# Optimization experiments

Hardware: AMD Instinct MI355X
Metric: run time of the kernel (lower is better)

Reference implementation:

```python
import jax, jax.numpy as jnp
import numpy as np

SIGMA = 0.1
B = 1.0
SPATIAL_WEIGHT = 0.5
EPS = 1e-5


def setup_inputs() -> dict:
    key = jax.random.key(0)
    k1, k2 = jax.random.split(key)
    N, C, H, W = 2, 256, 64, 64
    I_features = jax.random.normal(k1, (N, C, H, W), dtype=jnp.float32)
    T_features = jax.random.normal(k2, (N, C, H, W), dtype=jnp.float32)
    return {"I_features": I_features, "T_features": T_features}


def _calc_cx(raw):
    # raw: [N, P_T, H, W]; min + exp-softmax over the target-patch axis (axis=1)
    mn = jnp.min(raw, axis=1, keepdims=True)
    rel = raw / (mn + EPS)
    w = jnp.exp((B - rel) / SIGMA)
    return w / jnp.sum(w, axis=1, keepdims=True)


def reference(I_features, T_features):
    N, C, H, W = I_features.shape
    P = H * W

    # ---- spatial branch: L2 distances on a normalized meshgrid (C=2) ----
    rows = jnp.arange(H, dtype=jnp.float32) / (H + 1)
    cols = jnp.arange(W, dtype=jnp.float32) / (W + 1)
    grid = jnp.stack(jnp.meshgrid(rows, cols, indexing="ij"))  # [2, H, W]
    g = grid.reshape(2, P)                                      # [2, P]
    sq = jnp.sum(g * g, axis=0)                                 # [P]
    d = sq[:, None] + sq[None, :] - 2.0 * (g.T @ g)             # [P_I, P_T]
    d = jnp.clip(d, 0.0)
    raw_sp = d.T.reshape(1, P, H, W)  # [1, P_T, H, W]; identical per sample
    cx_sp = _calc_cx(raw_sp)

    # ---- feature branch: cosine similarity via centered, L2-normed feats ----
    meanT = jnp.mean(T_features, axis=(0, 2, 3), keepdims=True)
    Ic = I_features - meanT
    Tc = T_features - meanT
    In = Ic / jnp.linalg.norm(Ic, axis=1, keepdims=True)
    Tn = Tc / jnp.linalg.norm(Tc, axis=1, keepdims=True)
    Iv = In.reshape(N, C, P)
    Tv = Tn.reshape(N, C, P)
    dot = jnp.einsum("ncq,ncp->nqp", Tv, Iv)  # [N, P_T, P_I]
    raw_feat = ((1.0 - dot) / 2.0).reshape(N, P, H, W)
    cx_feat = _calc_cx(raw_feat)

    # ---- combine, max over I positions, mean over T patches, -log, mean ----
    cx = (1.0 - SPATIAL_WEIGHT) * cx_feat + SPATIAL_WEIGHT * cx_sp  # [N,P,H,W]
    m = jnp.max(cx, axis=(2, 3))  # [N, P]
    m = jnp.mean(m, axis=1)       # [N]
    return jnp.mean(-jnp.log(m))
```

## Files before the change

### kernel.cpp

```cpp
#include <hip/hip_runtime.h>
#include <math.h>

#define PP 4096
#define CC 256
#define NN 2
#define NSTEP 16

typedef __attribute__((ext_vector_type(4))) float f32x4;
typedef __attribute__((ext_vector_type(8))) int i32x8;

__device__ __forceinline__ void gld_lds16(const char* g, char* l) {
    __builtin_amdgcn_global_load_lds(
        (const __attribute__((address_space(1))) unsigned int*)g,
        (__attribute__((address_space(3))) unsigned int*)l, 16, 0, 0);
}


__global__ __launch_bounds__(256) void mean_kernel(const float* __restrict__ T,
                                                   float* __restrict__ meanT,
                                                   float* __restrict__ loss_acc) {
    int c = blockIdx.x, tid = threadIdx.x;
    float s = 0.f;
    for (int n = 0; n < NN; n++) {
        const float4* Tc = (const float4*)&T[(size_t)(n * CC + c) * PP];
        for (int g = 0; g < 4; g++) {
            float4 v = Tc[tid + g * 256];
            s += (v.x + v.y) + (v.z + v.w);
        }
    }
    __shared__ float red[256];
    red[tid] = s; __syncthreads();
    for (int st = 128; st > 0; st >>= 1) {
        if (tid < st) red[tid] += red[tid + st];
        __syncthreads();
    }
    if (tid == 0) meanT[c] = red[0] * (1.0f / (NN * PP));
    if (blockIdx.x == 0 && tid < NN) loss_acc[tid] = 0.f;
}

__global__ __launch_bounds__(256) void normalize_kernel(const float* __restrict__ I,
                                                        const float* __restrict__ T,
                                                        const float* __restrict__ meanT,
                                                        char* __restrict__ InT,
                                                        char* __restrict__ TnT) {
    int pc = blockIdx.x * 32;
    int n = blockIdx.y;
    int which = blockIdx.z;
    const float* X = which ? T : I;
    char* Y = which ? TnT : InT;

    __shared__ float tile[CC][36];
    __shared__ float red[32][32];
    __shared__ float invn[32];

    int tid = threadIdx.x;
    int pl4 = tid & 7, c0 = tid >> 3;
    float sq0 = 0.f, sq1 = 0.f, sq2 = 0.f, sq3 = 0.f;
    for (int c = c0; c < CC; c += 32) {
        float m = meanT[c];
        float4 v = *(const float4*)&X[(size_t)(n * CC + c) * PP + pc + pl4 * 4];
        v.x -= m; v.y -= m; v.z -= m; v.w -= m;
        *(float4*)&tile[c][pl4 * 4] = v;
        sq0 += v.x * v.x; sq1 += v.y * v.y; sq2 += v.z * v.z; sq3 += v.w * v.w;
    }
    red[c0][pl4 * 4 + 0] = sq0;
    red[c0][pl4 * 4 + 1] = sq1;
    red[c0][pl4 * 4 + 2] = sq2;
    red[c0][pl4 * 4 + 3] = sq3;
    __syncthreads();
    if (tid < 32) {
        float s = 0.f;
        for (int k = 0; k < 32; k++) s += red[k][tid];
        invn[tid] = 1.0f / sqrtf(s);
    }
    __syncthreads();
    for (int pass = 0; pass < 8; pass++) {
        int r = pass * 4 + (tid >> 6);
        int c4 = (tid & 63) * 4;
        float in = invn[r];
        float v0 = tile[c4 + 0][r] * in;
        float v1 = tile[c4 + 1][r] * in;
        float v2 = tile[c4 + 2][r] * in;
        float v3 = tile[c4 + 3][r] * in;
        int w = __builtin_amdgcn_cvt_pk_fp8_f32(v0, v1, 0, false);
        w = __builtin_amdgcn_cvt_pk_fp8_f32(v2, v3, w, true);
        *(unsigned*)&Y[(size_t)(n * PP + pc + r) * CC + c4] = (unsigned)w;
    }
}

__global__ __launch_bounds__(1024) void cx_strip(const char* __restrict__ TnT,
                                                 const char* __restrict__ InT,
                                                 float* __restrict__ loss_acc) {
    const int strip = blockIdx.x;
    const int n = blockIdx.y;
    const int p0 = strip * 32;
    const char* __restrict__ Ab = TnT + (size_t)n * PP * CC;
    const char* __restrict__ Bb = InT + (size_t)n * PP * CC + (size_t)p0 * CC;

    __shared__ __align__(16) char Aw[16][2][4096];
    __shared__ __align__(16) char Bsm[8192];
    __shared__ float redw[16][32];
    __shared__ float inv2s[32];
    __shared__ float dwl[32];

    const int tid = threadIdx.x;
    const int l = tid & 63, wv = tid >> 6;
    const int lm = l & 15, quad = l >> 4;
    const int lr4 = l >> 4;
    const int sl = l & 15;

    const char* asrc[4];
#pragma unroll
    for (int g = 0; g < 4; g++) {
        int row = g * 4 + lr4;
        asrc[g] = Ab + (size_t)(wv * 16 + row) * 256 + ((sl ^ (row & 15)) * 16);
    }
#define STAGE_A(qs, b)                                                        \
    {                                                                         \
        char* dbase_ = &Aw[wv][b][0];                                         \
        _Pragma("unroll")                                                     \
        for (int g_ = 0; g_ < 4; g_++)                                        \
            gld_lds16(asrc[g_] + (size_t)(qs) * 65536, dbase_ + g_ * 1024);   \
    }

    int aoff[8];
#pragma unroll
    for (int kb = 0; kb < 2; kb++)
#pragma unroll
        for (int j = 0; j < 4; j++)
            aoff[kb * 4 + j] = lm * 256 +
                (((kb * 8 + j * 2 + (quad >> 1)) ^ lm) * 16) + (quad & 1) * 8;

    if (wv < 8) {
        int rB = wv * 4 + lr4;
        gld_lds16(Bb + rB * 256 + ((sl ^ (rB & 15)) * 16), &Bsm[wv * 1024]);
    }
    STAGE_A(0, 0);
    __syncthreads();

    union BU { long l[2][8]; i32x8 v[2][2]; } bfu;
#pragma unroll
    for (int ct = 0; ct < 2; ct++)
#pragma unroll
        for (int ks = 0; ks < 8; ks++) {
            int g8 = ks * 4 + quad;
            int row = ct * 16 + lm;
            bfu.l[ct][ks] = *(const long*)&Bsm[row * 256 +
                             (((g8 >> 1) ^ (row & 15)) * 16) + (g8 & 1) * 8];
        }

    float amax[2] = {-3.4e38f, -3.4e38f};
    float hc[2] = {0.f, 0.f}, c0c[2] = {0.f, 0.f};
    float ss[2] = {0.f, 0.f};
    const int qdd0 = p0 >> 8, wdd0 = (p0 >> 4) & 15;
    const int qdd1 = (p0 + 16) >> 8, wdd1 = ((p0 + 16) >> 4) & 15;

#pragma unroll 1
    for (int pass = 0; pass < 2; pass++) {
        if (pass == 1) STAGE_A(0, 0);
#pragma unroll 1
        for (int qs = 0; qs < NSTEP; qs++) {
            if (qs < NSTEP - 1) {
                STAGE_A(qs + 1, (qs + 1) & 1);
                asm volatile("s_waitcnt vmcnt(4)" ::: "memory");
            } else {
                asm volatile("s_waitcnt vmcnt(0)" ::: "memory");
            }
            __builtin_amdgcn_sched_barrier(0);

            const char* Ac = &Aw[wv][qs & 1][0];
            f32x4 acc[2] = {};
#pragma unroll
            for (int kb = 0; kb < 2; kb++) {
                union AU { long l[4]; i32x8 v; } a_;
#pragma unroll
                for (int j = 0; j < 4; j++)
                    a_.l[j] = *(const long*)&Ac[aoff[kb * 4 + j]];
#pragma unroll
                for (int ct = 0; ct < 2; ct++)
                    acc[ct] = __builtin_amdgcn_mfma_scale_f32_16x16x128_f8f6f4(
                        a_.v, bfu.v[ct][kb], acc[ct],
                        0, 0,
                        0, 0x7f7f7f7f,
                        0, 0x7f7f7f7f);
            }
            if (pass == 0) {
#pragma unroll
                for (int ct = 0; ct < 2; ct++)
#pragma unroll
                    for (int e = 0; e < 4; e++)
                        amax[ct] = fmaxf(amax[ct], acc[ct][e]);
            } else {
#pragma unroll
                for (int ct = 0; ct < 2; ct++) {
                    float s2 = 0.f;
#pragma unroll
                    for (int e = 0; e < 4; e++)
                        s2 += exp2f(fmaf(acc[ct][e], hc[ct], c0c[ct]));
                    ss[ct] += s2;
                }
                if (qs == qdd0 && wv == wdd0 && quad == (lm >> 2))
                    dwl[lm] = exp2f(fmaf(acc[0][lm & 3], hc[0], c0c[0]));
                if (qs == qdd1 && wv == wdd1 && quad == (lm >> 2))
                    dwl[16 + lm] = exp2f(fmaf(acc[1][lm & 3], hc[1], c0c[1]));
            }
        }

        if (pass == 0) {
#pragma unroll
            for (int ct = 0; ct < 2; ct++) {
                amax[ct] = fmaxf(amax[ct], __shfl_xor(amax[ct], 16));
                amax[ct] = fmaxf(amax[ct], __shfl_xor(amax[ct], 32));
                if (quad == 0) redw[wv][ct * 16 + lm] = amax[ct];
            }
            __syncthreads();
            if (tid < 32) {
                float mx = redw[0][tid];
#pragma unroll
                for (int w2 = 1; w2 < 16; w2++) mx = fmaxf(mx, redw[w2][tid]);
                float mnv = (1.0f - mx) * 0.5f;
                inv2s[tid] = 14.4269504f / (mnv + 1e-5f);
            }
            __syncthreads();
            {
                float i20 = inv2s[lm], i21 = inv2s[16 + lm];
                hc[0] = i20 * 0.5f; c0c[0] = 14.4269504f - hc[0];
                hc[1] = i21 * 0.5f; c0c[1] = 14.4269504f - hc[1];
            }
        }
    }

#pragma unroll
    for (int ct = 0; ct < 2; ct++) {
        ss[ct] += __shfl_xor(ss[ct], 16);
        ss[ct] += __shfl_xor(ss[ct], 32);
        if (quad == 0) redw[wv][ct * 16 + lm] = ss[ct];
    }
    __syncthreads();
    if (tid < 32) {
        float s = 0.f;
#pragma unroll
        for (int w2 = 0; w2 < 16; w2++) s += redw[w2][tid];
        float part = dwl[tid] / s;
        part += __shfl_xor(part, 1);
        part += __shfl_xor(part, 2);
        part += __shfl_xor(part, 4);
        part += __shfl_xor(part, 8);
        part += __shfl_xor(part, 16);
        if (tid == 0) atomicAdd(&loss_acc[n], part);
    }
#undef STAGE_A
}

__global__ void finalize_kernel(const float* __restrict__ loss_acc,
                                float* __restrict__ out) {
    float m0 = 0.5f + 0.5f * (loss_acc[0] / (float)PP);
    float m1 = 0.5f + 0.5f * (loss_acc[1] / (float)PP);
    out[0] = 0.5f * (-logf(m0) - logf(m1));
}

extern "C" void kernel_launch(void* const* d_in, const int* in_sizes, int n_in,
                              void* d_out, int out_size, void* d_ws, size_t ws_size,
                              hipStream_t stream) {
    const float* I = (const float*)d_in[0];
    const float* T = (const float*)d_in[1];
    float* out = (float*)d_out;

    char* ws = (char*)d_ws;
    const size_t SZ_F8 = (size_t)NN * PP * CC;
    char* InT = ws;
    char* TnT = ws + SZ_F8;
    float* meanT = (float*)(ws + 2 * SZ_F8);
    float* loss_acc = (float*)(ws + 2 * SZ_F8 + 32768);

    mean_kernel<<<CC, 256, 0, stream>>>(T, meanT, loss_acc);
    normalize_kernel<<<dim3(PP / 32, NN, 2), 256, 0, stream>>>(I, T, meanT, InT, TnT);
    cx_strip<<<dim3(PP / 32, NN), 1024, 0, stream>>>(TnT, InT, loss_acc);
    finalize_kernel<<<1, 1, 0, stream>>>(loss_acc, out);
}
```

Before: 105.4 us.

## Load MFMA operands directly from global into registers, dropping LDS staging

Removes the LDS double-buffer staging of A and B tiles via global_load_lds, along with the swizzled LDS reads. Each lane now loads its fp8 operand fragments straight from global memory into registers and prefetches the next step's A fragment into a register double buffer. This cuts the LDS round trip, the explicit vmcnt waits and the LDS footprint, which may help occupancy. In exchange, global loads become 8-byte per-lane accesses with less coalescing, and loop-carried latency hiding is left to the compiler.

```diff
diff --git a/kernel.cpp b/kernel.cpp
--- a/kernel.cpp
+++ b/kernel.cpp
@@ -8,12 +8,7 @@
 
 typedef __attribute__((ext_vector_type(4))) float f32x4;
 typedef __attribute__((ext_vector_type(8))) int i32x8;
-
-__device__ __forceinline__ void gld_lds16(const char* g, char* l) {
-    __builtin_amdgcn_global_load_lds(
-        (const __attribute__((address_space(1))) unsigned int*)g,
-        (__attribute__((address_space(3))) unsigned int*)l, 16, 0, 0);
-}
+typedef __attribute__((ext_vector_type(2))) int i32x2;
 
 
 __global__ __launch_bounds__(256) void mean_kernel(const float* __restrict__ T,
@@ -97,8 +92,6 @@
     const char* __restrict__ Ab = TnT + (size_t)n * PP * CC;
     const char* __restrict__ Bb = InT + (size_t)n * PP * CC + (size_t)p0 * CC;
 
-    __shared__ __align__(16) char Aw[16][2][4096];
-    __shared__ __align__(16) char Bsm[8192];
     __shared__ float redw[16][32];
     __shared__ float inv2s[32];
     __shared__ float dwl[32];
@@ -106,48 +99,19 @@
     const int tid = threadIdx.x;
     const int l = tid & 63, wv = tid >> 6;
     const int lm = l & 15, quad = l >> 4;
-    const int lr4 = l >> 4;
-    const int sl = l & 15;
-
-    const char* asrc[4];
-#pragma unroll
-    for (int g = 0; g < 4; g++) {
-        int row = g * 4 + lr4;
-        asrc[g] = Ab + (size_t)(wv * 16 + row) * 256 + ((sl ^ (row & 15)) * 16);
-    }
-#define STAGE_A(qs, b)                                                        \
-    {                                                                         \
-        char* dbase_ = &Aw[wv][b][0];                                         \
-        _Pragma("unroll")                                                     \
-        for (int g_ = 0; g_ < 4; g_++)                                        \
-            gld_lds16(asrc[g_] + (size_t)(qs) * 65536, dbase_ + g_ * 1024);   \
-    }
-
-    int aoff[8];
-#pragma unroll
-    for (int kb = 0; kb < 2; kb++)
-#pragma unroll
-        for (int j = 0; j < 4; j++)
-            aoff[kb * 4 + j] = lm * 256 +
-                (((kb * 8 + j * 2 + (quad >> 1)) ^ lm) * 16) + (quad & 1) * 8;
-
-    if (wv < 8) {
-        int rB = wv * 4 + lr4;
-        gld_lds16(Bb + rB * 256 + ((sl ^ (rB & 15)) * 16), &Bsm[wv * 1024]);
-    }
-    STAGE_A(0, 0);
-    __syncthreads();
-
-    union BU { long l[2][8]; i32x8 v[2][2]; } bfu;
+
+    union BU { i32x2 d[2][2][4]; i32x8 v[2][2]; } bf;
 #pragma unroll
     for (int ct = 0; ct < 2; ct++)
 #pragma unroll
-        for (int ks = 0; ks < 8; ks++) {
-            int g8 = ks * 4 + quad;
-            int row = ct * 16 + lm;
-            bfu.l[ct][ks] = *(const long*)&Bsm[row * 256 +
-                             (((g8 >> 1) ^ (row & 15)) * 16) + (g8 & 1) * 8];
-        }
+        for (int kb = 0; kb < 2; kb++)
+#pragma unroll
+            for (int j = 0; j < 4; j++)
+                bf.d[ct][kb][j] = *(const i32x2*)(Bb + (ct * 16 + lm) * 256 +
+                                                  kb * 128 + j * 32 + quad * 8);
+
+    const char* Abase = Ab + (size_t)(wv * 16 + lm) * 256 + quad * 8;
+    union AU { i32x2 d[2][4]; i32x8 v[2]; };
 
     float amax[2] = {-3.4e38f, -3.4e38f};
     float hc[2] = {0.f, 0.f}, c0c[2] = {0.f, 0.f};
@@ -157,33 +121,35 @@
 
 #pragma unroll 1
     for (int pass = 0; pass < 2; pass++) {
-        if (pass == 1) STAGE_A(0, 0);
-#pragma unroll 1
+        AU cur, nxt;
+#pragma unroll
+        for (int kb = 0; kb < 2; kb++)
+#pragma unroll
+            for (int j = 0; j < 4; j++)
+                cur.d[kb][j] = *(const i32x2*)(Abase + kb * 128 + j * 32);
+
+#pragma unroll 2
         for (int qs = 0; qs < NSTEP; qs++) {
             if (qs < NSTEP - 1) {
-                STAGE_A(qs + 1, (qs + 1) & 1);
-                asm volatile("s_waitcnt vmcnt(4)" ::: "memory");
-            } else {
-                asm volatile("s_waitcnt vmcnt(0)" ::: "memory");
-            }
-            __builtin_amdgcn_sched_barrier(0);
-
-            const char* Ac = &Aw[wv][qs & 1][0];
+#pragma unroll
+                for (int kb = 0; kb < 2; kb++)
+#pragma unroll
+                    for (int j = 0; j < 4; j++)
+                        nxt.d[kb][j] = *(const i32x2*)(Abase +
+                            (size_t)(qs + 1) * 65536 + kb * 128 + j * 32);
+            }
+
             f32x4 acc[2] = {};
 #pragma unroll
-            for (int kb = 0; kb < 2; kb++) {
-                union AU { long l[4]; i32x8 v; } a_;
-#pragma unroll
-                for (int j = 0; j < 4; j++)
-                    a_.l[j] = *(const long*)&Ac[aoff[kb * 4 + j]];
+            for (int kb = 0; kb < 2; kb++)
 #pragma unroll
                 for (int ct = 0; ct < 2; ct++)
                     acc[ct] = __builtin_amdgcn_mfma_scale_f32_16x16x128_f8f6f4(
-                        a_.v, bfu.v[ct][kb], acc[ct],
+                        cur.v[kb], bf.v[ct][kb], acc[ct],
                         0, 0,
                         0, 0x7f7f7f7f,
                         0, 0x7f7f7f7f);
-            }
+
             if (pass == 0) {
 #pragma unroll
                 for (int ct = 0; ct < 2; ct++)
@@ -204,6 +170,8 @@
                 if (qs == qdd1 && wv == wdd1 && quad == (lm >> 2))
                     dwl[16 + lm] = exp2f(fmaf(acc[1][lm & 3], hc[1], c0c[1]));
             }
+
+            if (qs < NSTEP - 1) cur = nxt;
         }
 
         if (pass == 0) {
@@ -249,7 +217,6 @@
         part += __shfl_xor(part, 16);
         if (tid == 0) atomicAdd(&loss_acc[n], part);
     }
-#undef STAGE_A
 }
 
 __global__ void finalize_kernel(const float* __restrict__ loss_acc,
```

Result: slower. 192.7 us (+82.9%).
